# Performance work log

Measured on AMD Instinct MI355X. Metric: run time of the kernel, lower is better.

Reference implementation:

```python
import jax, jax.numpy as jnp
import numpy as np

SIM_RATIO = 0.5
TAU = 1e-4


def _gumbel_softmax_hard(logits, u, axis=-1):
    # torch F.gumbel_softmax(hard=True): straight-through one-hot
    eps = 1e-7
    g = -jnp.log(-jnp.log(u * (1.0 - 2.0 * eps) + eps))
    y_soft = jax.nn.softmax((logits + g) / TAU, axis=axis)
    idx = jnp.argmax(y_soft, axis=axis)
    y_hard = jax.nn.one_hot(idx, logits.shape[axis], dtype=y_soft.dtype)
    return y_hard - jax.lax.stop_gradient(y_soft) + y_soft


def setup_inputs() -> dict:
    key = jax.random.key(0)
    ks = jax.random.split(key, 7)
    N, S, n_items, n_users, d = 4096, 500, 100000, 50000, 64
    need_replace = jax.random.randint(ks[0], (N, 2), 0, n_users)  # user<n_users, item<n_users<=n_items ok
    union_feature = jax.random.normal(ks[1], (N, 2 * d), dtype=jnp.float32)
    all_items = jax.random.normal(ks[2], (n_items, d), dtype=jnp.float32)
    sample_items = jax.random.randint(ks[3], (n_users, S), 0, n_items)
    W = jax.random.normal(ks[4], (d, 2 * d), dtype=jnp.float32) * (1.0 / np.sqrt(2 * d))
    b = jax.random.normal(ks[5], (d,), dtype=jnp.float32) * 0.01
    gumbel_u = jax.random.uniform(ks[6], (N, S), dtype=jnp.float32)
    return {"need_replace": need_replace, "union_feature": union_feature,
            "all_items": all_items, "sample_items": sample_items,
            "W": W, "b": b, "gumbel_u": gumbel_u}


def reference(need_replace, union_feature, all_items, sample_items, W, b, gumbel_u):
    S = sample_items.shape[1]
    user_ids = need_replace[:, 0]
    item_ids = need_replace[:, 1]

    items_emb = all_items[item_ids][:, None, :]          # [N,1,d]
    samp = sample_items[user_ids]                        # [N,S]
    samp_feat = all_items[samp]                          # [N,S,d]

    rank_score = jnp.sum(items_emb * samp_feat, axis=-1)         # [N,S]
    item_ranking = jnp.argsort(rank_score, axis=1)               # ascending sort indices
    item_reverse = jnp.argsort(item_ranking, axis=1)             # rank of each candidate
    sample_item_sort = jnp.take_along_axis(samp, item_ranking, axis=1)  # [N,S]

    uif = union_feature @ W.T + b                                # [N,d]
    replace_score = jnp.sum(uif[:, None, :] * samp_feat, axis=-1)  # [N,S]

    rp = _gumbel_softmax_hard(replace_score, gumbel_u)           # [N,S] one-hot (ST)

    position_index = jnp.sum(item_reverse.astype(rp.dtype) * rp, axis=-1) + 1.0
    similarity = position_index / S
    # MarginLoss (assumed): mean absolute deviation from target ratio
    similarity_loss = jnp.mean(jnp.abs(similarity - SIM_RATIO))

    replaceable_items = jnp.sum(sample_item_sort.astype(rp.dtype) * rp, axis=-1).astype(jnp.int32)
    replaceable_items_feature = jnp.sum(samp_feat * rp[:, :, None], axis=1)  # [N,d]

    return replaceable_items, replaceable_items_feature, similarity_loss, jnp.mean(similarity)
```

## Files before the change

### kernel.cpp

```cpp
#include <hip/hip_runtime.h>

#define SDIM 500
#define DDIM 64
#define NT   256

__device__ __forceinline__ unsigned int ford(float x) {
    unsigned int u = __float_as_uint(x);
    return u ^ ((unsigned)((int)u >> 31) | 0x80000000u);
}

__global__ __launch_bounds__(NT) void rs_main(
    const int* __restrict__ need_replace,
    const float* __restrict__ union_feature,
    const float* __restrict__ all_items,
    const int* __restrict__ sample_items,
    const float* __restrict__ Wm,
    const float* __restrict__ bv,
    const float* __restrict__ gumbel_u,
    float* __restrict__ out_items,
    float* __restrict__ out_feat,
    float* __restrict__ ws_sim)
{
    __shared__ __align__(16) float s_uf[128];
    __shared__ __align__(16) float s_item[DDIM];
    __shared__ __align__(16) float s_uif[DDIM];
    __shared__ unsigned s_fv[SDIM];
    __shared__ float    s_key[SDIM];
    __shared__ int      s_samp[SDIM];
    __shared__ int      s_hist[256];
    __shared__ float    s_mv[4];
    __shared__ int      s_mi[4];
    __shared__ int      s_cnt4[4];
    __shared__ int      s_selb, s_selk, s_k, s_tn;
    __shared__ int      s_tbuf[64];

    const int n    = blockIdx.x;
    const int tid  = threadIdx.x;
    const int user = need_replace[2 * n];
    const int item = need_replace[2 * n + 1];

    if (tid < 128) s_uf[tid] = union_feature[(long)n * 128 + tid];
    else if (tid < 128 + DDIM) s_item[tid - 128] = all_items[(long)item * DDIM + (tid - 128)];
    const int* samp_row = sample_items + (long)user * SDIM;
    for (int s = tid; s < SDIM; s += NT) s_samp[s] = samp_row[s];
    __syncthreads();

    {
        const int row = tid >> 2, part = tid & 3;
        const float4* wr4 = (const float4*)(Wm + (long)row * 128);
        const float4* uf4 = (const float4*)s_uf;
        float acc = 0.f;
        #pragma unroll
        for (int q = 0; q < 8; ++q) {
            float4 w4 = wr4[part + q * 4];
            float4 u4 = uf4[part + q * 4];
            acc += w4.x * u4.x + w4.y * u4.y + w4.z * u4.z + w4.w * u4.w;
        }
        acc += __shfl_xor(acc, 1);
        acc += __shfl_xor(acc, 2);
        if (part == 0) s_uif[row] = acc + bv[row];
    }
    __syncthreads();

    {
        const int part = tid & 3, quad = tid >> 2;
        const float4* i4 = (const float4*)s_item + part * 4;
        const float4* u4 = (const float4*)s_uif + part * 4;
        const float4 wiA = i4[0], wiB = i4[1], wiC = i4[2], wiD = i4[3];
        const float4 wuA = u4[0], wuB = u4[1], wuC = u4[2], wuD = u4[3];
        for (int s0 = 0; s0 < SDIM; s0 += NT / 4) {
            int s = s0 + quad;
            float a0 = 0.f, a1 = 0.f;
            if (s < SDIM) {
                const float4* fr = (const float4*)(all_items + (long)s_samp[s] * DDIM) + part * 4;
                float4 f0 = fr[0], f1 = fr[1], f2 = fr[2], f3 = fr[3];
                a0 = f0.x*wiA.x + f0.y*wiA.y + f0.z*wiA.z + f0.w*wiA.w
                   + f1.x*wiB.x + f1.y*wiB.y + f1.z*wiB.z + f1.w*wiB.w
                   + f2.x*wiC.x + f2.y*wiC.y + f2.z*wiC.z + f2.w*wiC.w
                   + f3.x*wiD.x + f3.y*wiD.y + f3.z*wiD.z + f3.w*wiD.w;
                a1 = f0.x*wuA.x + f0.y*wuA.y + f0.z*wuA.z + f0.w*wuA.w
                   + f1.x*wuB.x + f1.y*wuB.y + f1.z*wuB.z + f1.w*wuB.w
                   + f2.x*wuC.x + f2.y*wuC.y + f2.z*wuC.z + f2.w*wuC.w
                   + f3.x*wuD.x + f3.y*wuD.y + f3.z*wuD.z + f3.w*wuD.w;
            }
            a0 += __shfl_xor(a0, 1); a0 += __shfl_xor(a0, 2);
            a1 += __shfl_xor(a1, 1); a1 += __shfl_xor(a1, 2);
            if (s < SDIM && part == 0) { s_fv[s] = ford(a0); s_key[s] = a1; }
        }
    }
    __syncthreads();

    const float* gu_row = gumbel_u + (long)n * SDIM;
    {
        float bvv = -__builtin_inff();
        int   bii = SDIM;
        for (int s = tid; s < SDIM; s += NT) {
            float u = gu_row[s];
            float g = -logf(-logf(u * (1.0f - 2e-7f) + 1e-7f));
            float v = s_key[s] + g;
            if (v > bvv) { bvv = v; bii = s; }
        }
        #pragma unroll
        for (int off = 1; off < 64; off <<= 1) {
            float v2 = __shfl_xor(bvv, off); int i2 = __shfl_xor(bii, off);
            if (v2 > bvv || (v2 == bvv && i2 < bii)) { bvv = v2; bii = i2; }
        }
        if ((tid & 63) == 0) { s_mv[tid >> 6] = bvv; s_mi[tid >> 6] = bii; }
        __syncthreads();
        if (tid == 0) {
            float mv = s_mv[0]; int mi = s_mi[0];
            for (int w = 1; w < 4; ++w) {
                float v2 = s_mv[w]; int i2 = s_mi[w];
                if (v2 > mv || (v2 == mv && i2 < mi)) { mv = v2; mi = i2; }
            }
            s_k = mi;
        }
        __syncthreads();
    }
    const int k = s_k;

    {
        const int src = s_samp[k];
        if (tid < DDIM)
            out_feat[(long)n * DDIM + tid] = all_items[(long)src * DDIM + tid];
    }

    int rank_k;
    {
        const unsigned fvk = s_fv[k];
        int cnt = 0;
        for (int s = tid; s < SDIM; s += NT) {
            unsigned v = s_fv[s];
            cnt += (int)((v < fvk) | ((v == fvk) & (s < k)));
        }
        #pragma unroll
        for (int off = 1; off < 64; off <<= 1) cnt += __shfl_xor(cnt, off);
        if ((tid & 63) == 0) s_cnt4[tid >> 6] = cnt;
        __syncthreads();
        rank_k = s_cnt4[0] + s_cnt4[1] + s_cnt4[2] + s_cnt4[3];
    }

    unsigned prefix = 0;
    int krem = k;
    for (int pass = 0; pass < 4; ++pass) {
        const int shift = 24 - 8 * pass;
        s_hist[tid] = 0;
        __syncthreads();
        const unsigned himask = pass ? (0xFFFFFFFFu << (shift + 8)) : 0u;
        for (int s = tid; s < SDIM; s += NT) {
            unsigned v = s_fv[s];
            if ((v & himask) == prefix) atomicAdd(&s_hist[(v >> shift) & 0xFF], 1);
        }
        __syncthreads();
        if (tid < 64) {
            int h0 = s_hist[4*tid], h1 = s_hist[4*tid+1], h2 = s_hist[4*tid+2], h3 = s_hist[4*tid+3];
            int s4 = h0 + h1 + h2 + h3, inc = s4;
            #pragma unroll
            for (int off = 1; off < 64; off <<= 1) {
                int t = __shfl_up(inc, off);
                if (tid >= off) inc += t;
            }
            int base = inc - s4;
            if (krem >= base && krem < inc) {
                if      (krem < base + h0)           { s_selb = 4*tid;   s_selk = krem - base; }
                else if (krem < base + h0 + h1)      { s_selb = 4*tid+1; s_selk = krem - base - h0; }
                else if (krem < base + h0 + h1 + h2) { s_selb = 4*tid+2; s_selk = krem - base - h0 - h1; }
                else                                 { s_selb = 4*tid+3; s_selk = krem - base - h0 - h1 - h2; }
            }
        }
        __syncthreads();
        prefix |= ((unsigned)s_selb) << shift;
        krem = s_selk;
        if (pass == 0) { if (tid == 0) s_tn = 0; }
    }

    __syncthreads();
    for (int s = tid; s < SDIM; s += NT) {
        if (s_fv[s] == prefix) {
            int slot = atomicAdd(&s_tn, 1);
            if (slot < 64) s_tbuf[slot] = s;
        }
    }
    __syncthreads();
    if (tid == 0) {
        int ntie = s_tn;
        int js = s_tbuf[0];
        if (ntie > 1) {
            for (int a = 0; a < ntie; ++a) {
                int c = s_tbuf[a], r = 0;
                for (int b2 = 0; b2 < ntie; ++b2) r += (int)(s_tbuf[b2] < c);
                if (r == krem) js = c;
            }
        }
        out_items[n] = (float)s_samp[js];
        ws_sim[n]    = (float)(rank_k + 1) / (float)SDIM;
    }
}

__global__ __launch_bounds__(NT) void rs_reduce(
    const float* __restrict__ ws_sim, float* __restrict__ out_scal, int N)
{
    __shared__ float s0[NT], s1[NT];
    int tid = threadIdx.x;
    float a = 0.f, m = 0.f;
    for (int i = tid; i < N; i += NT) {
        float sim = ws_sim[i];
        a += fabsf(sim - 0.5f);
        m += sim;
    }
    s0[tid] = a; s1[tid] = m;
    __syncthreads();
    for (int off = NT / 2; off > 0; off >>= 1) {
        if (tid < off) { s0[tid] += s0[tid + off]; s1[tid] += s1[tid + off]; }
        __syncthreads();
    }
    if (tid == 0) {
        out_scal[0] = s0[0] / (float)N;
        out_scal[1] = s1[0] / (float)N;
    }
}

extern "C" void kernel_launch(void* const* d_in, const int* in_sizes, int n_in,
                              void* d_out, int out_size, void* d_ws, size_t ws_size,
                              hipStream_t stream) {
    const int*   need_replace  = (const int*)d_in[0];
    const float* union_feature = (const float*)d_in[1];
    const float* all_items     = (const float*)d_in[2];
    const int*   sample_items  = (const int*)d_in[3];
    const float* Wm            = (const float*)d_in[4];
    const float* bv            = (const float*)d_in[5];
    const float* gumbel_u      = (const float*)d_in[6];

    const int N = in_sizes[0] / 2;

    float* out       = (float*)d_out;
    float* out_items = out;
    float* out_feat  = out + N;
    float* out_scal  = out + N + (long)N * DDIM;
    float* ws_sim    = (float*)d_ws;

    rs_main<<<N, NT, 0, stream>>>(need_replace, union_feature, all_items,
                                  sample_items, Wm, bv, gumbel_u,
                                  out_items, out_feat, ws_sim);
    rs_reduce<<<1, NT, 0, stream>>>(ws_sim, out_scal, N);
}
```

Measured before the change: 81.44 us.

## Replace 4-pass radix select with single 11-bit histogram pass and candidate ranking

```diff
diff --git a/kernel.cpp b/kernel.cpp
--- a/kernel.cpp
+++ b/kernel.cpp
@@ -3,13 +3,24 @@
 #define SDIM 500
 #define DDIM 64
 #define NT   256
-
-__device__ __forceinline__ unsigned int ford(float x) {
-    unsigned int u = __float_as_uint(x);
+#define HBITS  11
+#define HBINS  (1 << HBITS)
+#define HSHIFT (32 - HBITS)
+
+__device__ __forceinline__ unsigned ford(float x) {
+    unsigned u = __float_as_uint(x);
     return u ^ ((unsigned)((int)u >> 31) | 0x80000000u);
 }
 
-__global__ __launch_bounds__(NT) void rs_main(
+__device__ __forceinline__ float dot16(float4 a0, float4 a1, float4 a2, float4 a3,
+                                       float4 b0, float4 b1, float4 b2, float4 b3) {
+    return a0.x*b0.x + a0.y*b0.y + a0.z*b0.z + a0.w*b0.w
+         + a1.x*b1.x + a1.y*b1.y + a1.z*b1.z + a1.w*b1.w
+         + a2.x*b2.x + a2.y*b2.y + a2.z*b2.z + a2.w*b2.w
+         + a3.x*b3.x + a3.y*b3.y + a3.z*b3.z + a3.w*b3.w;
+}
+
+__global__ __launch_bounds__(NT, 6) void rs_main(
     const int* __restrict__ need_replace,
     const float* __restrict__ union_feature,
     const float* __restrict__ all_items,
@@ -19,34 +30,42 @@
     const float* __restrict__ gumbel_u,
     float* __restrict__ out_items,
     float* __restrict__ out_feat,
-    float* __restrict__ ws_sim)
+    int* __restrict__ ws_acc)
 {
     __shared__ __align__(16) float s_uf[128];
-    __shared__ __align__(16) float s_item[DDIM];
     __shared__ __align__(16) float s_uif[DDIM];
     __shared__ unsigned s_fv[SDIM];
     __shared__ float    s_key[SDIM];
     __shared__ int      s_samp[SDIM];
-    __shared__ int      s_hist[256];
-    __shared__ float    s_mv[4];
-    __shared__ int      s_mi[4];
-    __shared__ int      s_cnt4[4];
-    __shared__ int      s_selb, s_selk, s_k, s_tn;
-    __shared__ int      s_tbuf[64];
+    __shared__ union {
+        int hist[HBINS];
+        unsigned long long cand[SDIM];
+    } s_u;
+    __shared__ float s_mv[4];
+    __shared__ int   s_mi[4];
+    __shared__ int   s_cnt4[4];
+    __shared__ int   s_wt[4];
+    __shared__ int   s_k, s_selb, s_base, s_cn, s_jstar;
 
     const int n    = blockIdx.x;
     const int tid  = threadIdx.x;
+    const int wid  = tid >> 6;
+    const int lane = tid & 63;
+    const int part = tid & 3, quad = tid >> 2;
+
     const int user = need_replace[2 * n];
     const int item = need_replace[2 * n + 1];
+    const int*   samp_row = sample_items + (long)user * SDIM;
+    const float* gur      = gumbel_u + (long)n * SDIM;
 
     if (tid < 128) s_uf[tid] = union_feature[(long)n * 128 + tid];
-    else if (tid < 128 + DDIM) s_item[tid - 128] = all_items[(long)item * DDIM + (tid - 128)];
-    const int* samp_row = sample_items + (long)user * SDIM;
     for (int s = tid; s < SDIM; s += NT) s_samp[s] = samp_row[s];
-    __syncthreads();
-
-    {
-        const int row = tid >> 2, part = tid & 3;
+    const float4* ir = (const float4*)(all_items + (long)item * DDIM) + part * 4;
+    const float4 wiA = ir[0], wiB = ir[1], wiC = ir[2], wiD = ir[3];
+    __syncthreads();
+
+    {
+        const int row = quad;
         const float4* wr4 = (const float4*)(Wm + (long)row * 128);
         const float4* uf4 = (const float4*)s_uf;
         float acc = 0.f;
@@ -61,41 +80,41 @@
         if (part == 0) s_uif[row] = acc + bv[row];
     }
     __syncthreads();
-
-    {
-        const int part = tid & 3, quad = tid >> 2;
-        const float4* i4 = (const float4*)s_item + part * 4;
-        const float4* u4 = (const float4*)s_uif + part * 4;
-        const float4 wiA = i4[0], wiB = i4[1], wiC = i4[2], wiD = i4[3];
-        const float4 wuA = u4[0], wuB = u4[1], wuC = u4[2], wuD = u4[3];
-        for (int s0 = 0; s0 < SDIM; s0 += NT / 4) {
-            int s = s0 + quad;
-            float a0 = 0.f, a1 = 0.f;
-            if (s < SDIM) {
-                const float4* fr = (const float4*)(all_items + (long)s_samp[s] * DDIM) + part * 4;
-                float4 f0 = fr[0], f1 = fr[1], f2 = fr[2], f3 = fr[3];
-                a0 = f0.x*wiA.x + f0.y*wiA.y + f0.z*wiA.z + f0.w*wiA.w
-                   + f1.x*wiB.x + f1.y*wiB.y + f1.z*wiB.z + f1.w*wiB.w
-                   + f2.x*wiC.x + f2.y*wiC.y + f2.z*wiC.z + f2.w*wiC.w
-                   + f3.x*wiD.x + f3.y*wiD.y + f3.z*wiD.z + f3.w*wiD.w;
-                a1 = f0.x*wuA.x + f0.y*wuA.y + f0.z*wuA.z + f0.w*wuA.w
-                   + f1.x*wuB.x + f1.y*wuB.y + f1.z*wuB.z + f1.w*wuB.w
-                   + f2.x*wuC.x + f2.y*wuC.y + f2.z*wuC.z + f2.w*wuC.w
-                   + f3.x*wuD.x + f3.y*wuD.y + f3.z*wuD.z + f3.w*wuD.w;
-            }
-            a0 += __shfl_xor(a0, 1); a0 += __shfl_xor(a0, 2);
-            a1 += __shfl_xor(a1, 1); a1 += __shfl_xor(a1, 2);
-            if (s < SDIM && part == 0) { s_fv[s] = ford(a0); s_key[s] = a1; }
-        }
-    }
-    __syncthreads();
-
-    const float* gu_row = gumbel_u + (long)n * SDIM;
+    const float4* ur = (const float4*)s_uif + part * 4;
+    const float4 wuA = ur[0], wuB = ur[1], wuC = ur[2], wuD = ur[3];
+
+    float4 f0, f1, f2, f3;
+    {
+        const int idx0 = s_samp[quad];
+        const float4* p = (const float4*)(all_items + (long)idx0 * DDIM) + part * 4;
+        f0 = p[0]; f1 = p[1]; f2 = p[2]; f3 = p[3];
+    }
+    #pragma unroll
+    for (int i = 0; i < 8; ++i) {
+        const int s = i * 64 + quad;
+        float4 g0 = f0, g1 = f1, g2 = f2, g3 = f3;
+        if (i < 7) {
+            const int sn = s + 64;
+            const bool actn = (sn < SDIM);
+            const int idxn = s_samp[actn ? sn : 0];
+            const float4* q = (const float4*)(all_items + (long)idxn * DDIM) + part * 4;
+            if (actn) { g0 = q[0]; g1 = q[1]; g2 = q[2]; g3 = q[3]; }
+        }
+        const bool act = (s < SDIM);
+        float a0 = dot16(f0, f1, f2, f3, wiA, wiB, wiC, wiD);
+        float a1 = dot16(f0, f1, f2, f3, wuA, wuB, wuC, wuD);
+        a0 += __shfl_xor(a0, 1); a0 += __shfl_xor(a0, 2);
+        a1 += __shfl_xor(a1, 1); a1 += __shfl_xor(a1, 2);
+        if (act && part == 0) { s_fv[s] = ford(a0); s_key[s] = a1; }
+        f0 = g0; f1 = g1; f2 = g2; f3 = g3;
+    }
+    __syncthreads();
+
     {
         float bvv = -__builtin_inff();
         int   bii = SDIM;
         for (int s = tid; s < SDIM; s += NT) {
-            float u = gu_row[s];
+            float u = gur[s];
             float g = -logf(-logf(u * (1.0f - 2e-7f) + 1e-7f));
             float v = s_key[s] + g;
             if (v > bvv) { bvv = v; bii = s; }
@@ -105,10 +124,11 @@
             float v2 = __shfl_xor(bvv, off); int i2 = __shfl_xor(bii, off);
             if (v2 > bvv || (v2 == bvv && i2 < bii)) { bvv = v2; bii = i2; }
         }
-        if ((tid & 63) == 0) { s_mv[tid >> 6] = bvv; s_mi[tid >> 6] = bii; }
+        if (lane == 0) { s_mv[wid] = bvv; s_mi[wid] = bii; }
         __syncthreads();
         if (tid == 0) {
             float mv = s_mv[0]; int mi = s_mi[0];
+            #pragma unroll
             for (int w = 1; w < 4; ++w) {
                 float v2 = s_mv[w]; int i2 = s_mi[w];
                 if (v2 > mv || (v2 == mv && i2 < mi)) { mv = v2; mi = i2; }
@@ -125,98 +145,84 @@
             out_feat[(long)n * DDIM + tid] = all_items[(long)src * DDIM + tid];
     }
 
-    int rank_k;
-    {
-        const unsigned fvk = s_fv[k];
+    for (int h = tid; h < HBINS; h += NT) s_u.hist[h] = 0;
+    __syncthreads();
+    const unsigned fvk = s_fv[k];
+    {
         int cnt = 0;
         for (int s = tid; s < SDIM; s += NT) {
             unsigned v = s_fv[s];
             cnt += (int)((v < fvk) | ((v == fvk) & (s < k)));
+            atomicAdd(&s_u.hist[v >> HSHIFT], 1);
         }
         #pragma unroll
         for (int off = 1; off < 64; off <<= 1) cnt += __shfl_xor(cnt, off);
-        if ((tid & 63) == 0) s_cnt4[tid >> 6] = cnt;
+        if (lane == 0) s_cnt4[wid] = cnt;
+    }
+    __syncthreads();
+    const int rank_k = s_cnt4[0] + s_cnt4[1] + s_cnt4[2] + s_cnt4[3];
+
+    {
+        int b[8]; int p = 0;
+        #pragma unroll
+        for (int j = 0; j < 8; ++j) { b[j] = s_u.hist[tid * 8 + j]; p += b[j]; }
+        int inc = p;
+        #pragma unroll
+        for (int off = 1; off < 64; off <<= 1) {
+            int t = __shfl_up(inc, off);
+            if (lane >= off) inc += t;
+        }
+        if (lane == 63) s_wt[wid] = inc;
         __syncthreads();
-        rank_k = s_cnt4[0] + s_cnt4[1] + s_cnt4[2] + s_cnt4[3];
-    }
-
-    unsigned prefix = 0;
-    int krem = k;
-    for (int pass = 0; pass < 4; ++pass) {
-        const int shift = 24 - 8 * pass;
-        s_hist[tid] = 0;
-        __syncthreads();
-        const unsigned himask = pass ? (0xFFFFFFFFu << (shift + 8)) : 0u;
-        for (int s = tid; s < SDIM; s += NT) {
-            unsigned v = s_fv[s];
-            if ((v & himask) == prefix) atomicAdd(&s_hist[(v >> shift) & 0xFF], 1);
-        }
-        __syncthreads();
-        if (tid < 64) {
-            int h0 = s_hist[4*tid], h1 = s_hist[4*tid+1], h2 = s_hist[4*tid+2], h3 = s_hist[4*tid+3];
-            int s4 = h0 + h1 + h2 + h3, inc = s4;
-            #pragma unroll
-            for (int off = 1; off < 64; off <<= 1) {
-                int t = __shfl_up(inc, off);
-                if (tid >= off) inc += t;
-            }
-            int base = inc - s4;
-            if (krem >= base && krem < inc) {
-                if      (krem < base + h0)           { s_selb = 4*tid;   s_selk = krem - base; }
-                else if (krem < base + h0 + h1)      { s_selb = 4*tid+1; s_selk = krem - base - h0; }
-                else if (krem < base + h0 + h1 + h2) { s_selb = 4*tid+2; s_selk = krem - base - h0 - h1; }
-                else                                 { s_selb = 4*tid+3; s_selk = krem - base - h0 - h1 - h2; }
-            }
-        }
-        __syncthreads();
-        prefix |= ((unsigned)s_selb) << shift;
-        krem = s_selk;
-        if (pass == 0) { if (tid == 0) s_tn = 0; }
-    }
-
-    __syncthreads();
+        int wbase = 0;
+        for (int w = 0; w < wid; ++w) wbase += s_wt[w];
+        int run = wbase + inc - p;
+        #pragma unroll
+        for (int j = 0; j < 8; ++j) {
+            if (k >= run && k < run + b[j]) { s_selb = tid * 8 + j; s_base = run; }
+            run += b[j];
+        }
+    }
+    __syncthreads();
+    const int selb = s_selb;
+    const int kb   = k - s_base;
+    __syncthreads();
+    if (tid == 0) { s_cn = 0; s_jstar = -1; }
+    __syncthreads();
+
     for (int s = tid; s < SDIM; s += NT) {
-        if (s_fv[s] == prefix) {
-            int slot = atomicAdd(&s_tn, 1);
-            if (slot < 64) s_tbuf[slot] = s;
-        }
-    }
-    __syncthreads();
+        unsigned v = s_fv[s];
+        if ((int)(v >> HSHIFT) == selb) {
+            int slot = atomicAdd(&s_cn, 1);
+            s_u.cand[slot] = ((unsigned long long)v << 32) | (unsigned)s;
+        }
+    }
+    __syncthreads();
+    const int C = s_cn;
+
+    for (int i = tid; i < C; i += NT) {
+        unsigned long long w = s_u.cand[i];
+        int r = 0;
+        for (int j = 0; j < C; ++j) r += (int)(s_u.cand[j] < w);
+        if (r == kb) s_jstar = (int)(w & 0xffffffffu);
+    }
+    __syncthreads();
+
     if (tid == 0) {
-        int ntie = s_tn;
-        int js = s_tbuf[0];
-        if (ntie > 1) {
-            for (int a = 0; a < ntie; ++a) {
-                int c = s_tbuf[a], r = 0;
-                for (int b2 = 0; b2 < ntie; ++b2) r += (int)(s_tbuf[b2] < c);
-                if (r == krem) js = c;
-            }
-        }
-        out_items[n] = (float)s_samp[js];
-        ws_sim[n]    = (float)(rank_k + 1) / (float)SDIM;
-    }
-}
-
-__global__ __launch_bounds__(NT) void rs_reduce(
-    const float* __restrict__ ws_sim, float* __restrict__ out_scal, int N)
+        out_items[n] = (float)s_samp[s_jstar];
+        const int pos = rank_k + 1;
+        atomicAdd(&ws_acc[0], pos);
+        atomicAdd(&ws_acc[1], abs(pos - 250));
+    }
+}
+
+__global__ __launch_bounds__(64) void rs_fin(const int* __restrict__ ws_acc,
+                                             float* __restrict__ out_scal, int N)
 {
-    __shared__ float s0[NT], s1[NT];
-    int tid = threadIdx.x;
-    float a = 0.f, m = 0.f;
-    for (int i = tid; i < N; i += NT) {
-        float sim = ws_sim[i];
-        a += fabsf(sim - 0.5f);
-        m += sim;
-    }
-    s0[tid] = a; s1[tid] = m;
-    __syncthreads();
-    for (int off = NT / 2; off > 0; off >>= 1) {
-        if (tid < off) { s0[tid] += s0[tid + off]; s1[tid] += s1[tid + off]; }
-        __syncthreads();
-    }
-    if (tid == 0) {
-        out_scal[0] = s0[0] / (float)N;
-        out_scal[1] = s1[0] / (float)N;
+    if (threadIdx.x == 0) {
+        const double denom = (double)SDIM * (double)N;
+        out_scal[0] = (float)((double)ws_acc[1] / denom);
+        out_scal[1] = (float)((double)ws_acc[0] / denom);
     }
 }
 
@@ -237,10 +243,11 @@
     float* out_items = out;
     float* out_feat  = out + N;
     float* out_scal  = out + N + (long)N * DDIM;
-    float* ws_sim    = (float*)d_ws;
-
+    int*   ws_acc    = (int*)d_ws;
+
+    hipMemsetAsync(ws_acc, 0, 2 * sizeof(int), stream);
     rs_main<<<N, NT, 0, stream>>>(need_replace, union_feature, all_items,
                                   sample_items, Wm, bv, gumbel_u,
-                                  out_items, out_feat, ws_sim);
-    rs_reduce<<<1, NT, 0, stream>>>(ws_sim, out_scal, N);
-}
+                                  out_items, out_feat, ws_acc);
+    rs_fin<<<1, 64, 0, stream>>>(ws_acc, out_scal, N);
+}
```

After: 136.3 us. +67.3%, slower.
